# Performance work log

Measured on AMD Instinct MI355X. Metric: run time of the kernel, lower is better.

The kernel has to match this reference:

```python
import jax, jax.numpy as jnp
import numpy as np

B, L, H, N = 16, 4096, 256, 64
N2 = N // 2


def setup_inputs() -> dict:
    key = jax.random.key(0)
    ks = jax.random.split(key, 12)
    x = jax.random.normal(ks[0], (B, L, H), dtype=jnp.float32)
    # S4D kernel params (S4D-Lin init)
    log_dt = jax.random.uniform(ks[1], (H,), dtype=jnp.float32) * (
        np.log(0.1) - np.log(0.001)) + np.log(0.001)
    log_A_real = jnp.full((H, N2), jnp.log(0.5), dtype=jnp.float32)
    A_imag = jnp.broadcast_to(np.pi * jnp.arange(N2, dtype=jnp.float32), (H, N2)).copy()
    C_re = jax.random.normal(ks[2], (H, N2), dtype=jnp.float32) * (0.5 ** 0.5)
    C_im = jax.random.normal(ks[3], (H, N2), dtype=jnp.float32) * (0.5 ** 0.5)
    D = jax.random.normal(ks[4], (H,), dtype=jnp.float32)
    # LayerNorm + 2-layer MLP params
    ln_g = jnp.ones((H,), dtype=jnp.float32)
    ln_b = jnp.zeros((H,), dtype=jnp.float32)
    s = 1.0 / np.sqrt(H)
    W1 = jax.random.uniform(ks[5], (H, H), dtype=jnp.float32, minval=-s, maxval=s)
    b1 = jax.random.uniform(ks[6], (H,), dtype=jnp.float32, minval=-s, maxval=s)
    W2 = jax.random.uniform(ks[7], (H, H), dtype=jnp.float32, minval=-s, maxval=s)
    b2 = jax.random.uniform(ks[8], (H,), dtype=jnp.float32, minval=-s, maxval=s)
    return dict(x=x, log_dt=log_dt, log_A_real=log_A_real, A_imag=A_imag,
                C_re=C_re, C_im=C_im, D=D, ln_g=ln_g, ln_b=ln_b,
                W1=W1, b1=b1, W2=W2, b2=b2)


def _s4d_kernel(log_dt, log_A_real, A_imag, C_re, C_im, length):
    # Returns real convolution kernel of shape (H, length)
    dt = jnp.exp(log_dt)                                  # (H,)
    A = -jnp.exp(log_A_real) + 1j * A_imag                # (H, N2) complex
    C = (C_re + 1j * C_im).astype(jnp.complex64)
    dtA = A * dt[:, None]                                 # (H, N2)
    # Discretization (ZOH-like): C * (exp(dtA) - 1) / A
    Cd = C * (jnp.exp(dtA) - 1.0) / A                     # (H, N2)
    t = jnp.arange(length, dtype=jnp.float32)
    vand = jnp.exp(dtA[:, :, None] * t)                   # (H, N2, L) complex Vandermonde
    K = 2.0 * jnp.einsum('hn,hnl->hl', Cd, vand).real     # (H, L)
    return K


def _forward(x, log_dt, log_A_real, A_imag, C_re, C_im, D,
             ln_g, ln_b, W1, b1, W2, b2):
    Bsz, Lseq, Hdim = x.shape
    K = _s4d_kernel(log_dt, log_A_real, A_imag, C_re, C_im, Lseq)  # (H, L)
    u = jnp.transpose(x, (0, 2, 1))                       # (B, H, L)
    n_fft = 2 * Lseq
    k_f = jnp.fft.rfft(K, n=n_fft)                        # (H, n_fft//2+1)
    u_f = jnp.fft.rfft(u, n=n_fft)                        # (B, H, n_fft//2+1)
    y = jnp.fft.irfft(u_f * k_f, n=n_fft)[..., :Lseq]     # causal conv (B, H, L)
    y = y + u * D[None, :, None]                          # skip connection
    y = jnp.transpose(y, (0, 2, 1))                       # (B, L, H)
    # LayerNorm over H
    mu = jnp.mean(y, axis=-1, keepdims=True)
    var = jnp.mean(jnp.square(y - mu), axis=-1, keepdims=True)
    y = (y - mu) * jax.lax.rsqrt(var + 1e-5) * ln_g + ln_b
    # Linear -> ReLU -> Linear -> ReLU (dropout is identity in eval)
    y = jax.nn.relu(jnp.einsum('blh,oh->blo', y, W1) + b1)
    y = jax.nn.relu(jnp.einsum('blh,oh->blo', y, W2) + b2)
    return x + y


def reference(x, log_dt, log_A_real, A_imag, C_re, C_im, D,
              ln_g, ln_b, W1, b1, W2, b2):
    return _forward(x, log_dt, log_A_real, A_imag, C_re, C_im, D,
                    ln_g, ln_b, W1, b1, W2, b2)
```

## Files before the change

kernel.cpp:

```cpp
#include <hip/hip_runtime.h>

#define H_DIM 256
#define N2D   32
#define L_SEQ 4096
#define B_SZ  16
#define L_C   128
#define N_C   32
#define KPAD  136

typedef short short8 __attribute__((ext_vector_type(8)));
typedef short short4v __attribute__((ext_vector_type(4)));
typedef float f32x4  __attribute__((ext_vector_type(4)));
typedef unsigned short ushort;

__device__ __forceinline__ ushort f2bf(float f) {
  unsigned int u = __float_as_uint(f);
  u = (u + 0x7fffu + ((u >> 16) & 1u)) >> 16;
  return (ushort)u;
}
__device__ __forceinline__ float bf2f(ushort s) {
  return __uint_as_float(((unsigned int)s) << 16);
}

__global__ __launch_bounds__(128) void k_prep(
    const float* __restrict__ log_dt, const float* __restrict__ log_A_real,
    const float* __restrict__ A_imag, const float* __restrict__ C_re,
    const float* __restrict__ C_im, float* __restrict__ parK,
    ushort* __restrict__ Mb, ushort* __restrict__ Lb) {
  int h = blockIdx.x;
  int t = threadIdx.x;
  __shared__ float sdre[32], sdim[32], scdr[32], scdi[32], slr[32], sli[32];
  if (t < 32) {
    int i = h * 32 + t;
    float dt = expf(log_dt[h]);
    float ar = -expf(log_A_real[i]);
    float ai = A_imag[i];
    float dre = ar * dt, dim = ai * dt;
    float er = expf(dre), sn, cs;
    sincosf(dim, &sn, &cs);
    float lr = er * cs, li = er * sn;
    float nr = lr - 1.f, ni = li;
    float inv = 1.f / (ar * ar + ai * ai);
    float tr = (nr * ar + ni * ai) * inv, ti = (ni * ar - nr * ai) * inv;
    float cdr = C_re[i] * tr - C_im[i] * ti;
    float cdi = C_re[i] * ti + C_im[i] * tr;
    sdre[t] = dre; sdim[t] = dim; scdr[t] = cdr; scdi[t] = cdi;
    slr[t] = lr; sli[t] = li;
    float e1 = expf(128.f * dre), ph = 128.f * dim;
    sincosf(ph, &sn, &cs);
    parK[i] = e1 * cs;
    parK[8192 + i] = e1 * sn;
  }
  __syncthreads();
  float ksum = 0.f;
  float tf = (float)t;
  for (int n = 0; n < 32; ++n) {
    float e = expf(tf * sdre[n]);
    float sn, cs;
    sincosf(tf * sdim[n], &sn, &cs);
    float pr = e * cs, pi = e * sn;
    ksum = fmaf(scdr[n], pr, fmaf(-scdi[n], pi, ksum));
    Lb[((size_t)h * 64 + 2 * n) * 128 + (127 - t)] = f2bf(pr);
    Lb[((size_t)h * 64 + 2 * n + 1) * 128 + (127 - t)] = f2bf(pi);
    float plr = pr * slr[n] - pi * sli[n];
    float pli = pr * sli[n] + pi * slr[n];
    Mb[((size_t)h * 128 + t) * 64 + 2 * n] =
        f2bf(2.f * (scdr[n] * plr - scdi[n] * pli));
    Mb[((size_t)h * 128 + t) * 64 + 2 * n + 1] =
        f2bf(-2.f * (scdr[n] * pli + scdi[n] * plr));
  }
  parK[16384 + h * 128 + t] = 2.f * ksum;
}

__global__ void k_prep_T(const float* __restrict__ parK,
                         const float* __restrict__ Dp, ushort* __restrict__ T) {
  int idx = blockIdx.x * 256 + threadIdx.x;
  int h = idx >> 14;
  int rest = idx & 16383;
  int r = rest >> 7, j = rest & 127;
  int d = r - j;
  float v = 0.f;
  if (d >= 0) {
    v = parK[16384 + (h << 7) + d];
    if (d == 0) v += Dp[h];
  }
  T[idx] = f2bf(v);
}

__global__ __launch_bounds__(256) void k_wcomb(
    const float* __restrict__ W1, const float* __restrict__ W2,
    const float* __restrict__ gam, const float* __restrict__ bet,
    const float* __restrict__ b1, ushort* __restrict__ w1f,
    ushort* __restrict__ w2f, float* __restrict__ cs1,
    float* __restrict__ b1p) {
  __shared__ float ra[256], rb[256];
  if (blockIdx.x < 64) {
    int i = blockIdx.x * 256 + threadIdx.x;
    int mat = i >> 13;
    int fi = i & 8191;
    int l = fi & 63;
    int gk = fi >> 6;
    int g = gk & 15, kk = gk >> 4;
    int srow = g * 16 + (l & 15);
    int scol = kk * 32 + ((l >> 4) << 3);
    const float* W = mat ? W2 : W1;
    ushort* out = mat ? w2f : w1f;
    short8 v;
#pragma unroll
    for (int e = 0; e < 8; ++e) {
      float w = W[(size_t)srow * 256 + scol + e];
      if (!mat) w *= gam[scol + e];
      v[e] = (short)f2bf(w);
    }
    *(short8*)&out[(size_t)fi * 8] = v;
  } else {
    int o = blockIdx.x - 64, t = threadIdx.x;
    float w = W1[(size_t)o * 256 + t];
    ra[t] = bf2f(f2bf(w * gam[t]));
    rb[t] = w * bet[t];
    __syncthreads();
    for (int s = 128; s > 0; s >>= 1) {
      if (t < s) { ra[t] += ra[t + s]; rb[t] += rb[t + s]; }
      __syncthreads();
    }
    if (t == 0) { cs1[o] = ra[0]; b1p[o] = b1[o] + rb[0]; }
  }
}

__global__ __launch_bounds__(256) void k_xT(const float* __restrict__ x,
                                            ushort* __restrict__ U) {
  int blk = blockIdx.x;
  int b = blk >> 7;
  int l0 = (blk & 127) << 5;
  int t = threadIdx.x;
  __shared__ float tile[32][257];
#pragma unroll 8
  for (int r = 0; r < 32; ++r)
    tile[r][t] = x[((size_t)b * L_SEQ + l0 + r) * H_DIM + t];
  __syncthreads();
  int hq = t >> 2, ls = (t & 3) * 8;
#pragma unroll
  for (int pass = 0; pass < 4; ++pass) {
    int h = pass * 64 + hq;
    short8 v;
#pragma unroll
    for (int j = 0; j < 8; ++j) v[j] = (short)f2bf(tile[ls + j][h]);
    *(short8*)&U[(size_t)h * 65536 + (size_t)b * L_SEQ + l0 + ls] = v;
  }
}

__global__ __launch_bounds__(256, 2) void k_sy(
    const ushort* __restrict__ U, const ushort* __restrict__ Lb,
    const float* __restrict__ parK, const ushort* __restrict__ Mb,
    const ushort* __restrict__ T, ushort* __restrict__ Uo) {
  int wgid = (blockIdx.x & 7) * 128 + (blockIdx.x >> 3);
  int h = wgid >> 2, ct = wgid & 3;
  int t = threadIdx.x;
  int lane = t & 63, wid = t >> 6;
  int wm = wid & 1, wn = wid >> 1;
  int lr_ = lane & 15, lk = (lane >> 4) << 3;
  __shared__ ushort Bt[128][KPAD];
  __shared__ __attribute__((aligned(16))) ushort ovl[18432];
  ushort (*sts)[72] = (ushort(*)[72])ovl;
  ushort (*M_lds)[72] = (ushort(*)[72])(ovl + 128 * 72);
  ushort (*T_lds)[136] = (ushort(*)[136])ovl;
#pragma unroll
  for (int q = 0; q < 8; ++q) {
    int idx = q * 256 + t;
    int cc = idx >> 4, seg = idx & 15;
    int col = ct * 128 + cc;
    int b = col >> 5, c = col & 31;
    *(short8*)&Bt[cc][seg * 8] = *(const short8*)&U[
        (size_t)h * 65536 + (size_t)b * L_SEQ + c * L_C + seg * 8];
  }
#pragma unroll
  for (int q = 0; q < 4; ++q) {
    int idx = q * 256 + t;
    int r = idx >> 3, seg = idx & 7;
    *(short8*)&M_lds[r][seg * 8] =
        *(const short8*)&Mb[((size_t)h * 128 + r) * 64 + seg * 8];
  }
  __syncthreads();
  {
    f32x4 acc2[4][2];
#pragma unroll
    for (int m = 0; m < 4; ++m)
#pragma unroll
      for (int n = 0; n < 2; ++n) acc2[m][n] = (f32x4){0.f, 0.f, 0.f, 0.f};
#pragma unroll
    for (int ks = 0; ks < 4; ++ks) {
      int k0 = ks * 32;
      short8 a[4], bfr[2];
#pragma unroll
      for (int m = 0; m < 4; ++m)
        a[m] = *(const short8*)&Bt[wm * 64 + m * 16 + lr_][k0 + lk];
#pragma unroll
      for (int n = 0; n < 2; ++n)
        bfr[n] = *(const short8*)&Lb[
            ((size_t)h * 64 + wn * 32 + n * 16 + lr_) * 128 + k0 + lk];
#pragma unroll
      for (int m = 0; m < 4; ++m)
#pragma unroll
        for (int n = 0; n < 2; ++n)
          acc2[m][n] = __builtin_amdgcn_mfma_f32_16x16x32_bf16(
              a[m], bfr[n], acc2[m][n], 0, 0, 0);
    }
#pragma unroll
    for (int m = 0; m < 4; ++m)
#pragma unroll
      for (int n = 0; n < 2; ++n)
#pragma unroll
        for (int jj = 0; jj < 4; ++jj) {
          int rowl = wm * 64 + m * 16 + (lane >> 4) * 4 + jj;
          int col2n = wn * 32 + n * 16 + (lane & 15);
          sts[rowl][col2n] = f2bf(acc2[m][n][jj]);
        }
  }
  __syncthreads();
  if (t < 128) {
    int n = t & 31, bl = t >> 5;
    float Lr = parK[h * 32 + n], Li = parK[8192 + h * 32 + n];
    float cr = 0.f, ci = 0.f;
#pragma unroll
    for (int c = 0; c < N_C; ++c) {
      int rowl = bl * 32 + c;
      uint* p = (uint*)&sts[rowl][2 * n];
      uint v = *p;
      float fr = bf2f((ushort)(v & 0xffff));
      float fi = bf2f((ushort)(v >> 16));
      *p = (uint)f2bf(cr) | ((uint)f2bf(ci) << 16);
      float nr_ = fmaf(Lr, cr, fmaf(-Li, ci, fr));
      float ni_ = fmaf(Lr, ci, fmaf(Li, cr, fi));
      cr = nr_; ci = ni_;
    }
  }
  __syncthreads();
  f32x4 acc[4][4];
#pragma unroll
  for (int m = 0; m < 4; ++m)
#pragma unroll
    for (int n = 0; n < 4; ++n) acc[m][n] = (f32x4){0.f, 0.f, 0.f, 0.f};
#pragma unroll
  for (int ks = 0; ks < 2; ++ks) {
    int k0 = ks * 32;
    short8 a[4], bfr[4];
#pragma unroll
    for (int m = 0; m < 4; ++m)
      a[m] = *(const short8*)&sts[wm * 64 + m * 16 + lr_][k0 + lk];
#pragma unroll
    for (int n = 0; n < 4; ++n)
      bfr[n] = *(const short8*)&M_lds[wn * 64 + n * 16 + lr_][k0 + lk];
#pragma unroll
    for (int m = 0; m < 4; ++m)
#pragma unroll
      for (int n = 0; n < 4; ++n)
        acc[m][n] = __builtin_amdgcn_mfma_f32_16x16x32_bf16(a[m], bfr[n],
                                                            acc[m][n], 0, 0, 0);
  }
  __syncthreads();
#pragma unroll
  for (int q = 0; q < 8; ++q) {
    int idx = q * 256 + t;
    int r = idx >> 4, seg = idx & 15;
    *(short8*)&T_lds[r][seg * 8] =
        *(const short8*)&T[((size_t)h * 128 + r) * 128 + seg * 8];
  }
  __syncthreads();
#pragma unroll
  for (int ks = 0; ks < 4; ++ks) {
    int k0 = ks * 32;
    short8 a[4], bfr[4];
#pragma unroll
    for (int m = 0; m < 4; ++m)
      a[m] = *(const short8*)&Bt[wm * 64 + m * 16 + lr_][k0 + lk];
#pragma unroll
    for (int n = 0; n < 4; ++n)
      bfr[n] = *(const short8*)&T_lds[wn * 64 + n * 16 + lr_][k0 + lk];
#pragma unroll
    for (int m = 0; m < 4; ++m)
#pragma unroll
      for (int n = 0; n < 4; ++n)
        acc[m][n] = __builtin_amdgcn_mfma_f32_16x16x32_bf16(a[m], bfr[n],
                                                            acc[m][n], 0, 0, 0);
  }
  __syncthreads();
#pragma unroll
  for (int m = 0; m < 4; ++m) {
    int rowl = wm * 64 + m * 16 + (lane >> 4) * 4;
#pragma unroll
    for (int jj = 0; jj < 4; ++jj) {
      int row = rowl + jj;
#pragma unroll
      for (int n = 0; n < 4; ++n) {
        int lp = wn * 64 + n * 16 + (lane & 15);
        Bt[row][lp] = f2bf(acc[m][n][jj]);
      }
    }
  }
  __syncthreads();
#pragma unroll
  for (int q = 0; q < 8; ++q) {
    int idx = q * 256 + t;
    int r = idx >> 4, seg = idx & 15;
    int col = ct * 128 + r;
    int b = col >> 5, c = col & 31;
    *(short8*)&Uo[(size_t)h * 65536 + (size_t)b * L_SEQ + c * L_C + seg * 8] =
        *(const short8*)&Bt[r][seg * 8];
  }
}

__global__ __launch_bounds__(512, 4) void k_mlp(
    const ushort* __restrict__ U, const ushort* __restrict__ w1f,
    const ushort* __restrict__ w2f, const float* __restrict__ cs1,
    const float* __restrict__ b1p, const float* __restrict__ b2,
    const float* __restrict__ xres, float* __restrict__ outp) {
  int m0 = blockIdx.x << 7;
  int t = threadIdx.x;
  int lane = t & 63, wid = t >> 6;
  int wm = wid & 1, wn = wid >> 1;
  int lr_ = lane & 15, lk = (lane >> 4) << 3;
  __shared__ ushort smem[33792];
  __shared__ float redA[128][4], redB[128][4];
  __shared__ float mu_s[128], rs_s[128];
  {
    int hseg = t >> 4, l16 = t & 15;
    int sw = (l16 & 7) << 3;
#pragma unroll
    for (int p = 0; p < 8; ++p) {
      int h = p * 32 + hseg;
      short8 v = *(const short8*)&U[(size_t)h * 65536 + m0 + l16 * 8];
      int hx = h ^ sw;
#pragma unroll
      for (int e = 0; e < 8; ++e)
        smem[(l16 * 8 + e) * 264 + hx] = (ushort)v[e];
    }
  }
  __syncthreads();
  {
    int rl = t >> 2, q = (t & 3) << 6;
    float s = 0.f, s2 = 0.f;
#pragma unroll
    for (int e = 0; e < 64; e += 8) {
      short8 v = *(const short8*)&smem[rl * 264 + q + e];
#pragma unroll
      for (int j = 0; j < 8; ++j) {
        float f = bf2f((ushort)v[j]);
        s += f;
        s2 = fmaf(f, f, s2);
      }
    }
    redA[rl][t & 3] = s;
    redB[rl][t & 3] = s2;
  }
  __syncthreads();
  if (t < 128) {
    float ss = redA[t][0] + redA[t][1] + redA[t][2] + redA[t][3];
    float ss2 = redB[t][0] + redB[t][1] + redB[t][2] + redB[t][3];
    float mu = ss * (1.f / 256.f);
    float var = fmaf(ss2, 1.f / 256.f, -mu * mu);
    mu_s[t] = mu;
    rs_s[t] = rsqrtf(var + 1e-5f);
  }
  __syncthreads();
  f32x4 acc[4][4];
#pragma unroll
  for (int m = 0; m < 4; ++m)
#pragma unroll
    for (int n = 0; n < 4; ++n) acc[m][n] = (f32x4){0.f, 0.f, 0.f, 0.f};
#pragma unroll
  for (int kabs = 0; kabs < 8; ++kabs) {
    short8 af[4], bfr[4];
#pragma unroll
    for (int n = 0; n < 4; ++n)
      bfr[n] = *(const short8*)&w1f[(((size_t)kabs * 16 + wn * 4 + n) * 64 +
                                     lane) * 8];
#pragma unroll
    for (int m = 0; m < 4; ++m) {
      int row = wm * 64 + m * 16 + lr_;
      int sw = ((row >> 3) & 7) << 3;
      af[m] = *(const short8*)&smem[row * 264 + ((kabs * 32 + lk) ^ sw)];
    }
#pragma unroll
    for (int m = 0; m < 4; ++m)
#pragma unroll
      for (int n = 0; n < 4; ++n)
        acc[m][n] = __builtin_amdgcn_mfma_f32_16x16x32_bf16(af[m], bfr[n],
                                                            acc[m][n], 0, 0, 0);
  }
  __syncthreads();
  int prow = (lane >> 4) << 2;
  int pcol = lane & 15;
#pragma unroll
  for (int n = 0; n < 4; ++n) {
    int gcol = wn * 64 + n * 16 + pcol;
    float c1v = cs1[gcol], b1v = b1p[gcol];
#pragma unroll
    for (int m = 0; m < 4; ++m) {
      int rbase = wm * 64 + m * 16 + prow;
#pragma unroll
      for (int j = 0; j < 4; ++j) {
        int row = rbase + j;
        float v = fmaxf(
            fmaf(rs_s[row], acc[m][n][j] - mu_s[row] * c1v, b1v), 0.f);
        int byte = ((row << 9) + (gcol << 1)) ^ ((row & 7) << 4);
        smem[byte >> 1] = f2bf(v);
        acc[m][n][j] = 0.f;
      }
    }
  }
  __syncthreads();
#pragma unroll
  for (int kabs = 0; kabs < 8; ++kabs) {
    short8 af[4], bfr[4];
#pragma unroll
    for (int n = 0; n < 4; ++n)
      bfr[n] = *(const short8*)&w2f[(((size_t)kabs * 16 + wn * 4 + n) * 64 +
                                     lane) * 8];
#pragma unroll
    for (int m = 0; m < 4; ++m) {
      int row = wm * 64 + m * 16 + lr_;
      int byte = ((row << 9) + ((kabs * 32 + lk) << 1)) ^ ((row & 7) << 4);
      af[m] = *(const short8*)&smem[byte >> 1];
    }
#pragma unroll
    for (int m = 0; m < 4; ++m)
#pragma unroll
      for (int n = 0; n < 4; ++n)
        acc[m][n] = __builtin_amdgcn_mfma_f32_16x16x32_bf16(af[m], bfr[n],
                                                            acc[m][n], 0, 0, 0);
  }
  float bv2[4];
#pragma unroll
  for (int n = 0; n < 4; ++n) bv2[n] = b2[wn * 64 + n * 16 + pcol];
#pragma unroll
  for (int m = 0; m < 4; ++m) {
#pragma unroll
    for (int j = 0; j < 4; ++j) {
      int grow = m0 + wm * 64 + m * 16 + prow + j;
      size_t rb = (size_t)grow * 256;
#pragma unroll
      for (int n = 0; n < 4; ++n) {
        int gcol = wn * 64 + n * 16 + pcol;
        float v = fmaxf(acc[m][n][j] + bv2[n], 0.f);
        outp[rb + gcol] = xres[rb + gcol] + v;
      }
    }
  }
}

extern "C" void kernel_launch(void* const* d_in, const int* in_sizes, int n_in,
                              void* d_out, int out_size, void* d_ws, size_t ws_size,
                              hipStream_t stream) {
  const float* x          = (const float*)d_in[0];
  const float* log_dt     = (const float*)d_in[1];
  const float* log_A_real = (const float*)d_in[2];
  const float* A_imag     = (const float*)d_in[3];
  const float* C_re       = (const float*)d_in[4];
  const float* C_im       = (const float*)d_in[5];
  const float* Dp         = (const float*)d_in[6];
  const float* ln_g       = (const float*)d_in[7];
  const float* ln_b       = (const float*)d_in[8];
  const float* W1         = (const float*)d_in[9];
  const float* b1         = (const float*)d_in[10];
  const float* W2         = (const float*)d_in[11];
  const float* b2         = (const float*)d_in[12];

  char* ws = (char*)d_ws;
  float* parK = (float*)ws;
  float* cs1  = (float*)(ws + 0x30000);
  float* b1p  = (float*)(ws + 0x30400);
  ushort* w1f = (ushort*)(ws + 0x40000);
  ushort* w2f = (ushort*)(ws + 0x60000);
  ushort* Mb  = (ushort*)(ws + 0x80000);
  ushort* Lb  = (ushort*)(ws + 0x480000);
  ushort* Tb  = (ushort*)(ws + 0x880000);
  ushort* U   = (ushort*)(ws + 0x2080000);

  k_prep<<<256, 128, 0, stream>>>(log_dt, log_A_real, A_imag, C_re, C_im,
                                  parK, Mb, Lb);
  k_prep_T<<<16384, 256, 0, stream>>>(parK, Dp, Tb);
  k_wcomb<<<320, 256, 0, stream>>>(W1, W2, ln_g, ln_b, b1, w1f, w2f, cs1, b1p);
  k_xT<<<2048, 256, 0, stream>>>(x, U);
  k_sy<<<1024, 256, 0, stream>>>(U, Lb, parK, Mb, Tb, U);
  k_mlp<<<512, 512, 0, stream>>>(U, w1f, w2f, cs1, b1p, b2, x,
                                 (float*)d_out);
}
```

Measured before the change: 110.6 us.

## Merge prep kernels into one launch, build Toeplitz in LDS, vectorize MLP epilogue

The four front kernels (SSM parameter prep, weight packing, bias/colsum reduction, x transpose) are merged into a single launch that dispatches on block index. The 16384-block kernel that materialized the Toeplitz matrix in global memory is removed; k_sy now builds that tile in LDS from one kernel row plus D. The W2 packing permutes rows so the MLP epilogue can load bias and residual and store output as float4 vectors. This cuts launch count and global traffic, at the cost of extra per-block ALU work in k_sy and a remapped W2 layout that must match the epilogue indexing.

```diff
diff --git a/kernel.cpp b/kernel.cpp
--- a/kernel.cpp
+++ b/kernel.cpp
@@ -22,137 +22,124 @@
   return __uint_as_float(((unsigned int)s) << 16);
 }
 
-__global__ __launch_bounds__(128) void k_prep(
-    const float* __restrict__ log_dt, const float* __restrict__ log_A_real,
-    const float* __restrict__ A_imag, const float* __restrict__ C_re,
-    const float* __restrict__ C_im, float* __restrict__ parK,
-    ushort* __restrict__ Mb, ushort* __restrict__ Lb) {
-  int h = blockIdx.x;
-  int t = threadIdx.x;
-  __shared__ float sdre[32], sdim[32], scdr[32], scdi[32], slr[32], sli[32];
-  if (t < 32) {
-    int i = h * 32 + t;
-    float dt = expf(log_dt[h]);
-    float ar = -expf(log_A_real[i]);
-    float ai = A_imag[i];
-    float dre = ar * dt, dim = ai * dt;
-    float er = expf(dre), sn, cs;
-    sincosf(dim, &sn, &cs);
-    float lr = er * cs, li = er * sn;
-    float nr = lr - 1.f, ni = li;
-    float inv = 1.f / (ar * ar + ai * ai);
-    float tr = (nr * ar + ni * ai) * inv, ti = (ni * ar - nr * ai) * inv;
-    float cdr = C_re[i] * tr - C_im[i] * ti;
-    float cdi = C_re[i] * ti + C_im[i] * tr;
-    sdre[t] = dre; sdim[t] = dim; scdr[t] = cdr; scdi[t] = cdi;
-    slr[t] = lr; sli[t] = li;
-    float e1 = expf(128.f * dre), ph = 128.f * dim;
-    sincosf(ph, &sn, &cs);
-    parK[i] = e1 * cs;
-    parK[8192 + i] = e1 * sn;
-  }
-  __syncthreads();
-  float ksum = 0.f;
-  float tf = (float)t;
-  for (int n = 0; n < 32; ++n) {
-    float e = expf(tf * sdre[n]);
-    float sn, cs;
-    sincosf(tf * sdim[n], &sn, &cs);
-    float pr = e * cs, pi = e * sn;
-    ksum = fmaf(scdr[n], pr, fmaf(-scdi[n], pi, ksum));
-    Lb[((size_t)h * 64 + 2 * n) * 128 + (127 - t)] = f2bf(pr);
-    Lb[((size_t)h * 64 + 2 * n + 1) * 128 + (127 - t)] = f2bf(pi);
-    float plr = pr * slr[n] - pi * sli[n];
-    float pli = pr * sli[n] + pi * slr[n];
-    Mb[((size_t)h * 128 + t) * 64 + 2 * n] =
-        f2bf(2.f * (scdr[n] * plr - scdi[n] * pli));
-    Mb[((size_t)h * 128 + t) * 64 + 2 * n + 1] =
-        f2bf(-2.f * (scdr[n] * pli + scdi[n] * plr));
-  }
-  parK[16384 + h * 128 + t] = 2.f * ksum;
-}
-
-__global__ void k_prep_T(const float* __restrict__ parK,
-                         const float* __restrict__ Dp, ushort* __restrict__ T) {
-  int idx = blockIdx.x * 256 + threadIdx.x;
-  int h = idx >> 14;
-  int rest = idx & 16383;
-  int r = rest >> 7, j = rest & 127;
-  int d = r - j;
-  float v = 0.f;
-  if (d >= 0) {
-    v = parK[16384 + (h << 7) + d];
-    if (d == 0) v += Dp[h];
-  }
-  T[idx] = f2bf(v);
-}
-
-__global__ __launch_bounds__(256) void k_wcomb(
+__global__ __launch_bounds__(256) void k_front(
+    const float* __restrict__ x, const float* __restrict__ log_dt,
+    const float* __restrict__ log_A_real, const float* __restrict__ A_imag,
+    const float* __restrict__ C_re, const float* __restrict__ C_im,
     const float* __restrict__ W1, const float* __restrict__ W2,
     const float* __restrict__ gam, const float* __restrict__ bet,
-    const float* __restrict__ b1, ushort* __restrict__ w1f,
-    ushort* __restrict__ w2f, float* __restrict__ cs1,
-    float* __restrict__ b1p) {
-  __shared__ float ra[256], rb[256];
-  if (blockIdx.x < 64) {
-    int i = blockIdx.x * 256 + threadIdx.x;
-    int mat = i >> 13;
-    int fi = i & 8191;
-    int l = fi & 63;
-    int gk = fi >> 6;
-    int g = gk & 15, kk = gk >> 4;
-    int srow = g * 16 + (l & 15);
-    int scol = kk * 32 + ((l >> 4) << 3);
-    const float* W = mat ? W2 : W1;
-    ushort* out = mat ? w2f : w1f;
-    short8 v;
-#pragma unroll
-    for (int e = 0; e < 8; ++e) {
-      float w = W[(size_t)srow * 256 + scol + e];
-      if (!mat) w *= gam[scol + e];
-      v[e] = (short)f2bf(w);
-    }
-    *(short8*)&out[(size_t)fi * 8] = v;
+    const float* __restrict__ b1, float* __restrict__ parK,
+    ushort* __restrict__ Mb, ushort* __restrict__ Lb,
+    ushort* __restrict__ w1f, ushort* __restrict__ w2f,
+    float* __restrict__ cs1, float* __restrict__ b1p,
+    ushort* __restrict__ U) {
+  int bid = blockIdx.x;
+  int t = threadIdx.x;
+  if (bid < 256) {
+    int h = bid;
+    __shared__ float sdre[32], sdim[32], scdr[32], scdi[32], slr[32], sli[32];
+    if (t < 32) {
+      int i = h * 32 + t;
+      float dt = expf(log_dt[h]);
+      float ar = -expf(log_A_real[i]);
+      float ai = A_imag[i];
+      float dre = ar * dt, dim = ai * dt;
+      float er = expf(dre), sn, cs;
+      sincosf(dim, &sn, &cs);
+      float lr = er * cs, li = er * sn;
+      float nr = lr - 1.f, ni = li;
+      float inv = 1.f / (ar * ar + ai * ai);
+      float tr = (nr * ar + ni * ai) * inv, ti = (ni * ar - nr * ai) * inv;
+      float cdr = C_re[i] * tr - C_im[i] * ti;
+      float cdi = C_re[i] * ti + C_im[i] * tr;
+      sdre[t] = dre; sdim[t] = dim; scdr[t] = cdr; scdi[t] = cdi;
+      slr[t] = lr; sli[t] = li;
+      float e1 = expf(128.f * dre), ph = 128.f * dim;
+      sincosf(ph, &sn, &cs);
+      parK[i] = e1 * cs;
+      parK[8192 + i] = e1 * sn;
+    }
+    __syncthreads();
+    if (t < 128) {
+      float ksum = 0.f;
+      float tf = (float)t;
+      for (int n = 0; n < 32; ++n) {
+        float e = expf(tf * sdre[n]);
+        float sn, cs;
+        sincosf(tf * sdim[n], &sn, &cs);
+        float pr = e * cs, pi = e * sn;
+        ksum = fmaf(scdr[n], pr, fmaf(-scdi[n], pi, ksum));
+        Lb[((size_t)h * 64 + 2 * n) * 128 + (127 - t)] = f2bf(pr);
+        Lb[((size_t)h * 64 + 2 * n + 1) * 128 + (127 - t)] = f2bf(pi);
+        float plr = pr * slr[n] - pi * sli[n];
+        float pli = pr * sli[n] + pi * slr[n];
+        Mb[((size_t)h * 128 + t) * 64 + 2 * n] =
+            f2bf(2.f * (scdr[n] * plr - scdi[n] * pli));
+        Mb[((size_t)h * 128 + t) * 64 + 2 * n + 1] =
+            f2bf(-2.f * (scdr[n] * pli + scdi[n] * plr));
+      }
+      parK[16384 + h * 128 + t] = 2.f * ksum;
+    }
+  } else if (bid < 576) {
+    int wb = bid - 256;
+    if (wb < 64) {
+      int i = wb * 256 + t;
+      int mat = i >> 13;
+      int fi = i & 8191;
+      int l = fi & 63;
+      int gk = fi >> 6;
+      int g = gk & 15, kk = gk >> 4;
+      int srow = mat ? ((g >> 2) * 64 + (l & 15) * 4 + (g & 3))
+                     : (g * 16 + (l & 15));
+      int scol = kk * 32 + ((l >> 4) << 3);
+      const float* W = mat ? W2 : W1;
+      ushort* out = mat ? w2f : w1f;
+      short8 v;
+#pragma unroll
+      for (int e = 0; e < 8; ++e) {
+        float w = W[(size_t)srow * 256 + scol + e];
+        if (!mat) w *= gam[scol + e];
+        v[e] = (short)f2bf(w);
+      }
+      *(short8*)&out[(size_t)fi * 8] = v;
+    } else {
+      int o = wb - 64;
+      __shared__ float ra[256], rb[256];
+      float w = W1[(size_t)o * 256 + t];
+      ra[t] = bf2f(f2bf(w * gam[t]));
+      rb[t] = w * bet[t];
+      __syncthreads();
+      for (int s = 128; s > 0; s >>= 1) {
+        if (t < s) { ra[t] += ra[t + s]; rb[t] += rb[t + s]; }
+        __syncthreads();
+      }
+      if (t == 0) { cs1[o] = ra[0]; b1p[o] = b1[o] + rb[0]; }
+    }
   } else {
-    int o = blockIdx.x - 64, t = threadIdx.x;
-    float w = W1[(size_t)o * 256 + t];
-    ra[t] = bf2f(f2bf(w * gam[t]));
-    rb[t] = w * bet[t];
+    int blk = bid - 576;
+    int b = blk >> 7;
+    int l0 = (blk & 127) << 5;
+    __shared__ float tile[32][257];
+#pragma unroll 8
+    for (int r = 0; r < 32; ++r)
+      tile[r][t] = x[((size_t)b * L_SEQ + l0 + r) * H_DIM + t];
     __syncthreads();
-    for (int s = 128; s > 0; s >>= 1) {
-      if (t < s) { ra[t] += ra[t + s]; rb[t] += rb[t + s]; }
-      __syncthreads();
-    }
-    if (t == 0) { cs1[o] = ra[0]; b1p[o] = b1[o] + rb[0]; }
-  }
-}
-
-__global__ __launch_bounds__(256) void k_xT(const float* __restrict__ x,
-                                            ushort* __restrict__ U) {
-  int blk = blockIdx.x;
-  int b = blk >> 7;
-  int l0 = (blk & 127) << 5;
-  int t = threadIdx.x;
-  __shared__ float tile[32][257];
-#pragma unroll 8
-  for (int r = 0; r < 32; ++r)
-    tile[r][t] = x[((size_t)b * L_SEQ + l0 + r) * H_DIM + t];
-  __syncthreads();
-  int hq = t >> 2, ls = (t & 3) * 8;
-#pragma unroll
-  for (int pass = 0; pass < 4; ++pass) {
-    int h = pass * 64 + hq;
-    short8 v;
-#pragma unroll
-    for (int j = 0; j < 8; ++j) v[j] = (short)f2bf(tile[ls + j][h]);
-    *(short8*)&U[(size_t)h * 65536 + (size_t)b * L_SEQ + l0 + ls] = v;
+    int hq = t >> 2, ls = (t & 3) * 8;
+#pragma unroll
+    for (int pass = 0; pass < 4; ++pass) {
+      int h = pass * 64 + hq;
+      short8 v;
+#pragma unroll
+      for (int j = 0; j < 8; ++j) v[j] = (short)f2bf(tile[ls + j][h]);
+      *(short8*)&U[(size_t)h * 65536 + (size_t)b * L_SEQ + l0 + ls] = v;
+    }
   }
 }
 
 __global__ __launch_bounds__(256, 2) void k_sy(
     const ushort* __restrict__ U, const ushort* __restrict__ Lb,
     const float* __restrict__ parK, const ushort* __restrict__ Mb,
-    const ushort* __restrict__ T, ushort* __restrict__ Uo) {
+    const float* __restrict__ Dp, ushort* __restrict__ Uo) {
   int wgid = (blockIdx.x & 7) * 128 + (blockIdx.x >> 3);
   int h = wgid >> 2, ct = wgid & 3;
   int t = threadIdx.x;
@@ -161,9 +148,15 @@
   int lr_ = lane & 15, lk = (lane >> 4) << 3;
   __shared__ ushort Bt[128][KPAD];
   __shared__ __attribute__((aligned(16))) ushort ovl[18432];
+  __shared__ float Krow[128];
   ushort (*sts)[72] = (ushort(*)[72])ovl;
   ushort (*M_lds)[72] = (ushort(*)[72])(ovl + 128 * 72);
   ushort (*T_lds)[136] = (ushort(*)[136])ovl;
+  if (t < 128) {
+    float kv = parK[16384 + h * 128 + t];
+    if (t == 0) kv += Dp[h];
+    Krow[t] = kv;
+  }
 #pragma unroll
   for (int q = 0; q < 8; ++q) {
     int idx = q * 256 + t;
@@ -262,8 +255,14 @@
   for (int q = 0; q < 8; ++q) {
     int idx = q * 256 + t;
     int r = idx >> 4, seg = idx & 15;
-    *(short8*)&T_lds[r][seg * 8] =
-        *(const short8*)&T[((size_t)h * 128 + r) * 128 + seg * 8];
+    short8 v;
+#pragma unroll
+    for (int e = 0; e < 8; ++e) {
+      int d = r - (seg * 8 + e);
+      float f = (d >= 0) ? Krow[d] : 0.f;
+      v[e] = (short)f2bf(f);
+    }
+    *(short8*)&T_lds[r][seg * 8] = v;
   }
   __syncthreads();
 #pragma unroll
@@ -429,21 +428,19 @@
         acc[m][n] = __builtin_amdgcn_mfma_f32_16x16x32_bf16(af[m], bfr[n],
                                                             acc[m][n], 0, 0, 0);
   }
-  float bv2[4];
-#pragma unroll
-  for (int n = 0; n < 4; ++n) bv2[n] = b2[wn * 64 + n * 16 + pcol];
+  f32x4 bv2q = *(const f32x4*)&b2[wn * 64 + pcol * 4];
 #pragma unroll
   for (int m = 0; m < 4; ++m) {
 #pragma unroll
     for (int j = 0; j < 4; ++j) {
       int grow = m0 + wm * 64 + m * 16 + prow + j;
-      size_t rb = (size_t)grow * 256;
-#pragma unroll
-      for (int n = 0; n < 4; ++n) {
-        int gcol = wn * 64 + n * 16 + pcol;
-        float v = fmaxf(acc[m][n][j] + bv2[n], 0.f);
-        outp[rb + gcol] = xres[rb + gcol] + v;
-      }
+      size_t base = (size_t)grow * 256 + wn * 64 + pcol * 4;
+      f32x4 xr = *(const f32x4*)&xres[base];
+      f32x4 o;
+#pragma unroll
+      for (int n = 0; n < 4; ++n)
+        o[n] = xr[n] + fmaxf(acc[m][n][j] + bv2q[n], 0.f);
+      *(f32x4*)&outp[base] = o;
     }
   }
 }
@@ -473,15 +470,12 @@
   ushort* w2f = (ushort*)(ws + 0x60000);
   ushort* Mb  = (ushort*)(ws + 0x80000);
   ushort* Lb  = (ushort*)(ws + 0x480000);
-  ushort* Tb  = (ushort*)(ws + 0x880000);
   ushort* U   = (ushort*)(ws + 0x2080000);
 
-  k_prep<<<256, 128, 0, stream>>>(log_dt, log_A_real, A_imag, C_re, C_im,
-                                  parK, Mb, Lb);
-  k_prep_T<<<16384, 256, 0, stream>>>(parK, Dp, Tb);
-  k_wcomb<<<320, 256, 0, stream>>>(W1, W2, ln_g, ln_b, b1, w1f, w2f, cs1, b1p);
-  k_xT<<<2048, 256, 0, stream>>>(x, U);
-  k_sy<<<1024, 256, 0, stream>>>(U, Lb, parK, Mb, Tb, U);
+  k_front<<<2624, 256, 0, stream>>>(x, log_dt, log_A_real, A_imag, C_re, C_im,
+                                    W1, W2, ln_g, ln_b, b1, parK, Mb, Lb,
+                                    w1f, w2f, cs1, b1p, U);
+  k_sy<<<1024, 256, 0, stream>>>(U, Lb, parK, Mb, Dp, U);
   k_mlp<<<512, 512, 0, stream>>>(U, w1f, w2f, cs1, b1p, b2, x,
                                  (float*)d_out);
 }
```

Result: faster. 93.41 us, median of 4 (-15.5%).
